# Kernel tuning notes

Measured on AMD Instinct MI355X. Metric: run time of the kernel, lower is better.

Reference implementation:

```python
import jax, jax.numpy as jnp
import numpy as np

B, H, W, C = 8, 128, 128, 384
WS, SHIFT, NH = 8, 4, 12
N = WS * WS            # tokens per window = 64
HD = C // NH           # head dim = 32
SCALE = HD ** -0.5


def _rel_pos_index():
    ch, cw = np.meshgrid(np.arange(WS), np.arange(WS), indexing='ij')
    cf = np.stack([ch.ravel(), cw.ravel()])            # (2, N)
    rel = cf[:, :, None] - cf[:, None, :]              # (2, N, N)
    rel = rel.transpose(1, 2, 0)                       # (N, N, 2)
    rel[:, :, 0] += WS - 1
    rel[:, :, 1] += WS - 1
    rel[:, :, 0] *= 2 * WS - 1
    return jnp.asarray(rel.sum(-1))                    # (N, N) int

REL_IDX = _rel_pos_index()


def _shift_mask():
    # standard Swin SW-MSA mask, built once with numpy
    img = np.zeros((1, H, W, 1), np.float32)
    cnt = 0
    for hs in (slice(0, -WS), slice(-WS, -SHIFT), slice(-SHIFT, None)):
        for ws_ in (slice(0, -WS), slice(-WS, -SHIFT), slice(-SHIFT, None)):
            img[:, hs, ws_, :] = cnt
            cnt += 1
    m = img.reshape(1, H // WS, WS, W // WS, WS, 1).transpose(0, 1, 3, 2, 4, 5)
    m = m.reshape(-1, N)                               # (nW, N)
    am = m[:, None, :] - m[:, :, None]                 # (nW, N, N)
    return np.where(am != 0, np.float32(-100.0), np.float32(0.0))


def _ln(x, g, b, eps=1e-5):
    mu = x.mean(-1, keepdims=True)
    var = ((x - mu) ** 2).mean(-1, keepdims=True)
    return (x - mu) * jax.lax.rsqrt(var + eps) * g + b


def setup_inputs() -> dict:
    key = jax.random.key(0)
    ks = jax.random.split(key, 10)
    s = 0.02
    return {
        'x': jax.random.normal(ks[0], (B, H * W, C), jnp.float32),
        'qkv_w': jax.random.normal(ks[1], (3 * C, C), jnp.float32) * s,
        'qkv_b': jnp.zeros((3 * C,), jnp.float32),
        'proj_w': jax.random.normal(ks[2], (C, C), jnp.float32) * s,
        'proj_b': jnp.zeros((C,), jnp.float32),
        'rel_bias_table': jax.random.normal(ks[3], ((2 * WS - 1) ** 2, NH), jnp.float32) * s,
        'g1': jnp.ones((C,), jnp.float32), 'b1': jnp.zeros((C,), jnp.float32),
        'g2': jnp.ones((C,), jnp.float32), 'b2': jnp.zeros((C,), jnp.float32),
        'fc1_w': jax.random.normal(ks[4], (4 * C, C), jnp.float32) * s,
        'fc1_b': jnp.zeros((4 * C,), jnp.float32),
        'fc2_w': jax.random.normal(ks[5], (C, 4 * C), jnp.float32) * s,
        'fc2_b': jnp.zeros((C,), jnp.float32),
        'attn_mask': jnp.asarray(_shift_mask()),       # (nW, N, N)
    }


def reference(x, qkv_w, qkv_b, proj_w, proj_b, rel_bias_table, g1, b1, g2, b2,
              fc1_w, fc1_b, fc2_w, fc2_b, attn_mask):
    shortcut = x
    h = _ln(x, g1, b1).reshape(B, H, W, C)
    # cyclic shift (SW-MSA)
    h = jnp.roll(h, (-SHIFT, -SHIFT), axis=(1, 2))
    # window partition -> (B*nW, N, C)
    nWh, nWw = H // WS, W // WS
    hw = h.reshape(B, nWh, WS, nWw, WS, C).transpose(0, 1, 3, 2, 4, 5)
    hw = hw.reshape(B * nWh * nWw, N, C)
    # qkv projection
    qkv = jnp.einsum('bnc,dc->bnd', hw, qkv_w) + qkv_b   # (Bw, N, 3C)
    qkv = qkv.reshape(-1, N, 3, NH, HD).transpose(2, 0, 3, 1, 4)
    q, k, v = qkv[0], qkv[1], qkv[2]                    # (Bw, NH, N, HD)
    attn = jnp.einsum('bhnd,bhmd->bhnm', q * SCALE, k)  # (Bw, NH, N, N)
    bias = rel_bias_table[REL_IDX.reshape(-1)].reshape(N, N, NH)
    attn = attn + bias.transpose(2, 0, 1)[None]
    # shift mask: attn viewed as (B, nW, NH, N, N) + mask (nW, 1, N, N)
    nW = nWh * nWw
    attn = attn.reshape(B, nW, NH, N, N) + attn_mask[None, :, None]
    attn = jax.nn.softmax(attn.reshape(-1, NH, N, N), axis=-1)
    out = jnp.einsum('bhnm,bhmd->bnhd', attn, v).reshape(-1, N, C)
    out = jnp.einsum('bnc,dc->bnd', out, proj_w) + proj_b
    # window reverse + un-shift
    out = out.reshape(B, nWh, nWw, WS, WS, C).transpose(0, 1, 3, 2, 4, 5)
    out = out.reshape(B, H, W, C)
    out = jnp.roll(out, (SHIFT, SHIFT), axis=(1, 2)).reshape(B, H * W, C)
    x = shortcut + out
    # MLP block
    h2 = _ln(x, g2, b2)
    h2 = jax.nn.gelu(jnp.einsum('blc,dc->bld', h2, fc1_w) + fc1_b, approximate=False)
    h2 = jnp.einsum('bld,cd->blc', h2, fc2_w) + fc2_b
    return x + h2
```

## Files before the change

### kernel.cpp

```cpp
#include <hip/hip_runtime.h>
#include <hip/hip_bf16.h>
#include <math.h>

typedef __attribute__((ext_vector_type(4))) float f32x4;
typedef __attribute__((ext_vector_type(8))) short bf16x8;

__device__ __forceinline__ unsigned short f2bf(float f) {
  unsigned int x = __builtin_bit_cast(unsigned int, f);
  x += 0x7fffu + ((x >> 16) & 1u);
  return (unsigned short)(x >> 16);
}

__device__ __forceinline__ void gload_lds16(const void* g, void* l) {
  __builtin_amdgcn_global_load_lds(
      (const __attribute__((address_space(1))) unsigned int*)g,
      (__attribute__((address_space(3))) unsigned int*)l, 16, 0, 0);
}

__global__ void cvt_f32_bf16(const float* __restrict__ s, unsigned short* __restrict__ d, int n) {
  int i = blockIdx.x * 256 + threadIdx.x;
  if (i < n) d[i] = f2bf(s[i]);
}

template <int REMAP>
__global__ __launch_bounds__(256)
void ln_kernel(const float* __restrict__ x, const float* __restrict__ g,
               const float* __restrict__ b, unsigned short* __restrict__ dst_o) {
  int r = blockIdx.x * 4 + (threadIdx.x >> 6);
  int lane = threadIdx.x & 63;
  size_t src;
  if (REMAP) {
    int w = r >> 6, t = r & 63;
    int bb = w >> 8, wi = (w >> 4) & 15, wj = w & 15;
    int i = t >> 3, j = t & 7;
    int p = (wi * 8 + i + 4) & 127, q = (wj * 8 + j + 4) & 127;
    src = ((size_t)bb * 16384 + p * 128 + q) * 384;
  } else {
    src = (size_t)r * 384;
  }
  float v[6];
  float s = 0.f, s2 = 0.f;
#pragma unroll
  for (int m = 0; m < 6; ++m) {
    v[m] = x[src + lane + 64 * m];
    s += v[m];
    s2 += v[m] * v[m];
  }
#pragma unroll
  for (int o2 = 1; o2 < 64; o2 <<= 1) {
    s += __shfl_xor(s, o2);
    s2 += __shfl_xor(s2, o2);
  }
  float mu = s * (1.f / 384.f);
  float var = s2 * (1.f / 384.f) - mu * mu;
  float ri = rsqrtf(var + 1e-5f);
  size_t dst = (size_t)r * 384;
#pragma unroll
  for (int m = 0; m < 6; ++m) {
    int c = lane + 64 * m;
    dst_o[dst + c] = f2bf((v[m] - mu) * ri * g[c] + b[c]);
  }
}

template <int EPI>
__global__ __launch_bounds__(256, 2)
void gemm_bt(const unsigned short* __restrict__ A, const unsigned short* __restrict__ Bw,
             const float* __restrict__ bias, int M, int N, int K,
             unsigned short* __restrict__ Obf, const float* __restrict__ resid,
             float* __restrict__ Of) {
  __shared__ unsigned short smA[128 * 64];
  __shared__ unsigned short smB[128 * 64];
  const int tid = threadIdx.x;
  const int lane = tid & 63;
  const int wid = tid >> 6;
  const int wm = wid >> 1, wn = wid & 1;
  const int li = lane & 15, lg = lane >> 4;
  const int m0 = blockIdx.y * 128;
  const int n0 = blockIdx.x * 128;

  f32x4 acc[4][4] = {};

  const int srow = wid * 32 + (lane >> 3);
  const int scol = (lane & 7) * 8;
  const unsigned short* gA = A + (size_t)(m0 + srow) * K + scol;
  const unsigned short* gB = Bw + (size_t)(n0 + srow) * K + scol;

  for (int k0 = 0; k0 < K; k0 += 64) {
#pragma unroll
    for (int c = 0; c < 4; ++c) {
      gload_lds16(gA + (size_t)(c * 8) * K + k0, &smA[(wid * 32 + c * 8) * 64]);
      gload_lds16(gB + (size_t)(c * 8) * K + k0, &smB[(wid * 32 + c * 8) * 64]);
    }
    __syncthreads();
#pragma unroll
    for (int kk = 0; kk < 2; ++kk) {
      bf16x8 a[4], bb[4];
#pragma unroll
      for (int f = 0; f < 4; ++f) {
        a[f] = *(const bf16x8*)&smA[(wm * 64 + f * 16 + li) * 64 + kk * 32 + lg * 8];
        bb[f] = *(const bf16x8*)&smB[(wn * 64 + f * 16 + li) * 64 + kk * 32 + lg * 8];
      }
#pragma unroll
      for (int mf = 0; mf < 4; ++mf)
#pragma unroll
        for (int nf = 0; nf < 4; ++nf)
          acc[mf][nf] = __builtin_amdgcn_mfma_f32_16x16x32_bf16(a[mf], bb[nf], acc[mf][nf], 0, 0, 0);
    }
    __syncthreads();
  }

#pragma unroll
  for (int mf = 0; mf < 4; ++mf) {
#pragma unroll
    for (int r = 0; r < 4; ++r) {
      int mrow = m0 + wm * 64 + mf * 16 + lg * 4 + r;
      size_t orow = (size_t)mrow;
      if (EPI == 2) {
        int w = mrow >> 6, t = mrow & 63;
        int bb2 = w >> 8, wi = (w >> 4) & 15, wj = w & 15;
        int i = t >> 3, j = t & 7;
        int p = (wi * 8 + i + 4) & 127, q = (wj * 8 + j + 4) & 127;
        orow = (size_t)bb2 * 16384 + p * 128 + q;
      }
#pragma unroll
      for (int nf = 0; nf < 4; ++nf) {
        int col = n0 + wn * 64 + nf * 16 + li;
        float v = acc[mf][nf][r] + bias[col];
        if (EPI == 0) {
          Obf[(size_t)mrow * N + col] = f2bf(v);
        } else if (EPI == 1) {
          float gl = 0.5f * v * (1.f + erff(v * 0.70710678118654752f));
          Obf[(size_t)mrow * N + col] = f2bf(gl);
        } else if (EPI == 2) {
          Of[orow * 384 + col] = v + resid[orow * 384 + col];
        } else {
          Of[(size_t)mrow * N + col] = v + resid[(size_t)mrow * N + col];
        }
      }
    }
  }
}

__global__ __launch_bounds__(256, 2)
void attn_kernel(const unsigned short* __restrict__ qkv, const float* __restrict__ btab,
                 const float* __restrict__ mask, unsigned short* __restrict__ out) {
  __shared__ unsigned short v_lds[4][64 * 40];
  __shared__ unsigned short p_lds[4][64 * 72];
  const int w = blockIdx.x;
  const int tid = threadIdx.x;
  const int wid = tid >> 6, lane = tid & 63;
  const int li = lane & 15, lg = lane >> 4;
  const float* mrow = mask + (size_t)(w & 255) * 4096;
  const size_t base = (size_t)w * 64;
  const float SC = 0.17677669529663688f;

#pragma unroll 1
  for (int hi = 0; hi < 3; ++hi) {
    int h = wid * 3 + hi;
    bf16x8 aq[4], bk[4];
#pragma unroll
    for (int f = 0; f < 4; ++f) {
      size_t off = (base + f * 16 + li) * 1152 + h * 32 + lg * 8;
      aq[f] = *(const bf16x8*)&qkv[off];
      bk[f] = *(const bf16x8*)&qkv[off + 384];
    }
    f32x4 s[4][4] = {};
#pragma unroll
    for (int mf = 0; mf < 4; ++mf)
#pragma unroll
      for (int nf = 0; nf < 4; ++nf)
        s[mf][nf] = __builtin_amdgcn_mfma_f32_16x16x32_bf16(aq[mf], bk[nf], s[mf][nf], 0, 0, 0);

    {
      const unsigned short* vp = &qkv[(base + lane) * 1152 + 768 + h * 32];
      unsigned short* dp = &v_lds[wid][lane * 40];
#pragma unroll
      for (int c = 0; c < 4; ++c) *(bf16x8*)&dp[c * 8] = *(const bf16x8*)&vp[c * 8];
    }

#pragma unroll
    for (int mf = 0; mf < 4; ++mf) {
#pragma unroll
      for (int r = 0; r < 4; ++r) {
        int m = mf * 16 + lg * 4 + r;
        float mx = -1e30f;
#pragma unroll
        for (int nf = 0; nf < 4; ++nf) {
          int n = nf * 16 + li;
          int ridx = ((m >> 3) - (n >> 3) + 7) * 15 + (m & 7) - (n & 7) + 7;
          float val = s[mf][nf][r] * SC + btab[ridx * 12 + h] + mrow[m * 64 + n];
          s[mf][nf][r] = val;
          mx = fmaxf(mx, val);
        }
#pragma unroll
        for (int o2 = 1; o2 < 16; o2 <<= 1) mx = fmaxf(mx, __shfl_xor(mx, o2));
        float sum = 0.f;
#pragma unroll
        for (int nf = 0; nf < 4; ++nf) {
          float e = __expf(s[mf][nf][r] - mx);
          s[mf][nf][r] = e;
          sum += e;
        }
#pragma unroll
        for (int o2 = 1; o2 < 16; o2 <<= 1) sum += __shfl_xor(sum, o2);
        float inv = 1.f / sum;
#pragma unroll
        for (int nf = 0; nf < 4; ++nf) s[mf][nf][r] *= inv;
      }
    }

#pragma unroll
    for (int mf = 0; mf < 4; ++mf)
#pragma unroll
      for (int nf = 0; nf < 4; ++nf)
#pragma unroll
        for (int r = 0; r < 4; ++r) {
          int m = mf * 16 + lg * 4 + r, n = nf * 16 + li;
          p_lds[wid][m * 72 + n] = f2bf(s[mf][nf][r]);
        }

    f32x4 o[4][2] = {};
#pragma unroll
    for (int kf = 0; kf < 2; ++kf) {
      bf16x8 bv[2];
#pragma unroll
      for (int df = 0; df < 2; ++df) {
        bf16x8 t;
#pragma unroll
        for (int e = 0; e < 8; ++e)
          t[e] = (short)v_lds[wid][(kf * 32 + lg * 8 + e) * 40 + df * 16 + li];
        bv[df] = t;
      }
#pragma unroll
      for (int mf = 0; mf < 4; ++mf) {
        bf16x8 pa = *(const bf16x8*)&p_lds[wid][(mf * 16 + li) * 72 + kf * 32 + lg * 8];
#pragma unroll
        for (int df = 0; df < 2; ++df)
          o[mf][df] = __builtin_amdgcn_mfma_f32_16x16x32_bf16(pa, bv[df], o[mf][df], 0, 0, 0);
      }
    }

#pragma unroll
    for (int mf = 0; mf < 4; ++mf)
#pragma unroll
      for (int df = 0; df < 2; ++df)
#pragma unroll
        for (int r = 0; r < 4; ++r) {
          size_t row = base + mf * 16 + lg * 4 + r;
          out[row * 384 + h * 32 + df * 16 + li] = f2bf(o[mf][df][r]);
        }
  }
}

extern "C" void kernel_launch(void* const* d_in, const int* in_sizes, int n_in,
                              void* d_out, int out_size, void* d_ws, size_t ws_size,
                              hipStream_t stream) {
  const float* x      = (const float*)d_in[0];
  const float* qkv_w  = (const float*)d_in[1];
  const float* qkv_b  = (const float*)d_in[2];
  const float* proj_w = (const float*)d_in[3];
  const float* proj_b = (const float*)d_in[4];
  const float* rel    = (const float*)d_in[5];
  const float* g1     = (const float*)d_in[6];
  const float* b1     = (const float*)d_in[7];
  const float* g2     = (const float*)d_in[8];
  const float* b2     = (const float*)d_in[9];
  const float* fc1_w  = (const float*)d_in[10];
  const float* fc1_b  = (const float*)d_in[11];
  const float* fc2_w  = (const float*)d_in[12];
  const float* fc2_b  = (const float*)d_in[13];
  const float* mask   = (const float*)d_in[14];
  float* out = (float*)d_out;
  char* ws = (char*)d_ws;

  const int M = 131072;
  unsigned short* hw     = (unsigned short*)ws;
  unsigned short* qkv    = (unsigned short*)(ws + 100663296);
  unsigned short* hmid   = (unsigned short*)ws;
  unsigned short* attn_o = (unsigned short*)(ws + 402653184);
  unsigned short* ln2o   = attn_o;
  float*          x1     = (float*)(ws + 503316480);
  unsigned short* wq     = (unsigned short*)(ws + 704643072);
  unsigned short* wp     = wq + 442368;
  unsigned short* w1     = wp + 147456;
  unsigned short* w2     = w1 + 589824;

  cvt_f32_bf16<<<(442368 + 255) / 256, 256, 0, stream>>>(qkv_w, wq, 442368);
  cvt_f32_bf16<<<(147456 + 255) / 256, 256, 0, stream>>>(proj_w, wp, 147456);
  cvt_f32_bf16<<<(589824 + 255) / 256, 256, 0, stream>>>(fc1_w, w1, 589824);
  cvt_f32_bf16<<<(589824 + 255) / 256, 256, 0, stream>>>(fc2_w, w2, 589824);

  ln_kernel<1><<<M / 4, 256, 0, stream>>>(x, g1, b1, hw);

  gemm_bt<0><<<dim3(9, 1024), 256, 0, stream>>>(hw, wq, qkv_b, M, 1152, 384, qkv, nullptr, nullptr);

  attn_kernel<<<2048, 256, 0, stream>>>(qkv, rel, mask, attn_o);

  gemm_bt<2><<<dim3(3, 1024), 256, 0, stream>>>(attn_o, wp, proj_b, M, 384, 384, nullptr, x, x1);

  ln_kernel<0><<<M / 4, 256, 0, stream>>>(x1, g2, b2, ln2o);

  gemm_bt<1><<<dim3(12, 1024), 256, 0, stream>>>(ln2o, w1, fc1_b, M, 1536, 384, hmid, nullptr, nullptr);

  gemm_bt<3><<<dim3(3, 1024), 256, 0, stream>>>(hmid, w2, fc2_b, M, 384, 1536, nullptr, x1, out);
}
```

Measured before the change: 1.272 ms.

## Double-buffer A tiles, read weights directly from global, remap blocks per XCD

The GEMM kernel now double-buffers only the activation tile in LDS, prefetching the next K slice while computing the current one. Weight fragments are loaded straight from global memory (through cache) instead of being staged in LDS. Launches become 1D, with the block index remapped so consecutive tiles land on the same XCD for L2 reuse. Occupancy is raised to 4 blocks/CU. There is a risk: the loop body no longer shows a __syncthreads between prefetch and compute, so buffer hazards may exist, and direct global B loads may add latency.

```diff
diff --git a/kernel.cpp b/kernel.cpp
--- a/kernel.cpp
+++ b/kernel.cpp
@@ -63,43 +63,59 @@
 }
 
 template <int EPI>
-__global__ __launch_bounds__(256, 2)
+__global__ __launch_bounds__(256, 4)
 void gemm_bt(const unsigned short* __restrict__ A, const unsigned short* __restrict__ Bw,
-             const float* __restrict__ bias, int M, int N, int K,
+             const float* __restrict__ bias, int M, int N, int K, int NT,
              unsigned short* __restrict__ Obf, const float* __restrict__ resid,
              float* __restrict__ Of) {
-  __shared__ unsigned short smA[128 * 64];
-  __shared__ unsigned short smB[128 * 64];
+  __shared__ unsigned short smA[2][128 * 64];
   const int tid = threadIdx.x;
   const int lane = tid & 63;
   const int wid = tid >> 6;
   const int wm = wid >> 1, wn = wid & 1;
   const int li = lane & 15, lg = lane >> 4;
-  const int m0 = blockIdx.y * 128;
-  const int n0 = blockIdx.x * 128;
-
-  f32x4 acc[4][4] = {};
+
+  const int nwg = gridDim.x;
+  const int orig = blockIdx.x;
+  const int q = nwg >> 3, r = nwg & 7;
+  const int xcd = orig & 7, loc = orig >> 3;
+  const int wg = (xcd < r ? xcd * (q + 1) : r * (q + 1) + (xcd - r) * q) + loc;
+  const int m0 = (wg / NT) * 128;
+  const int n0 = (wg % NT) * 128;
 
   const int srow = wid * 32 + (lane >> 3);
   const int scol = (lane & 7) * 8;
   const unsigned short* gA = A + (size_t)(m0 + srow) * K + scol;
-  const unsigned short* gB = Bw + (size_t)(n0 + srow) * K + scol;
-
-  for (int k0 = 0; k0 < K; k0 += 64) {
-#pragma unroll
-    for (int c = 0; c < 4; ++c) {
-      gload_lds16(gA + (size_t)(c * 8) * K + k0, &smA[(wid * 32 + c * 8) * 64]);
-      gload_lds16(gB + (size_t)(c * 8) * K + k0, &smB[(wid * 32 + c * 8) * 64]);
-    }
-    __syncthreads();
+  const unsigned short* gB[4];
+#pragma unroll
+  for (int nf = 0; nf < 4; ++nf)
+    gB[nf] = Bw + (size_t)(n0 + wn * 64 + nf * 16 + li) * K + lg * 8;
+
+  f32x4 acc[4][4] = {};
+  const int nk = K >> 6;
+
+#pragma unroll
+  for (int c = 0; c < 4; ++c)
+    gload_lds16(gA + (size_t)(c * 8) * K, &smA[0][(wid * 32 + c * 8) * 64]);
+  __syncthreads();
+
+  for (int k0 = 0; k0 < nk; ++k0) {
+    const int cur = k0 & 1;
+    if (k0 + 1 < nk) {
+#pragma unroll
+      for (int c = 0; c < 4; ++c)
+        gload_lds16(gA + (size_t)(c * 8) * K + (k0 + 1) * 64,
+                    &smA[cur ^ 1][(wid * 32 + c * 8) * 64]);
+    }
 #pragma unroll
     for (int kk = 0; kk < 2; ++kk) {
       bf16x8 a[4], bb[4];
 #pragma unroll
-      for (int f = 0; f < 4; ++f) {
-        a[f] = *(const bf16x8*)&smA[(wm * 64 + f * 16 + li) * 64 + kk * 32 + lg * 8];
-        bb[f] = *(const bf16x8*)&smB[(wn * 64 + f * 16 + li) * 64 + kk * 32 + lg * 8];
-      }
+      for (int f = 0; f < 4; ++f)
+        a[f] = *(const bf16x8*)&smA[cur][(wm * 64 + f * 16 + li) * 64 + kk * 32 + lg * 8];
+#pragma unroll
+      for (int f = 0; f < 4; ++f)
+        bb[f] = *(const bf16x8*)&gB[f][(size_t)(k0 * 64 + kk * 32)];
 #pragma unroll
       for (int mf = 0; mf < 4; ++mf)
 #pragma unroll
@@ -112,20 +128,20 @@
 #pragma unroll
   for (int mf = 0; mf < 4; ++mf) {
 #pragma unroll
-    for (int r = 0; r < 4; ++r) {
-      int mrow = m0 + wm * 64 + mf * 16 + lg * 4 + r;
+    for (int r2 = 0; r2 < 4; ++r2) {
+      int mrow = m0 + wm * 64 + mf * 16 + lg * 4 + r2;
       size_t orow = (size_t)mrow;
       if (EPI == 2) {
         int w = mrow >> 6, t = mrow & 63;
         int bb2 = w >> 8, wi = (w >> 4) & 15, wj = w & 15;
         int i = t >> 3, j = t & 7;
-        int p = (wi * 8 + i + 4) & 127, q = (wj * 8 + j + 4) & 127;
-        orow = (size_t)bb2 * 16384 + p * 128 + q;
+        int p = (wi * 8 + i + 4) & 127, qq = (wj * 8 + j + 4) & 127;
+        orow = (size_t)bb2 * 16384 + p * 128 + qq;
       }
 #pragma unroll
       for (int nf = 0; nf < 4; ++nf) {
         int col = n0 + wn * 64 + nf * 16 + li;
-        float v = acc[mf][nf][r] + bias[col];
+        float v = acc[mf][nf][r2] + bias[col];
         if (EPI == 0) {
           Obf[(size_t)mrow * N + col] = f2bf(v);
         } else if (EPI == 1) {
@@ -292,15 +308,15 @@
 
   ln_kernel<1><<<M / 4, 256, 0, stream>>>(x, g1, b1, hw);
 
-  gemm_bt<0><<<dim3(9, 1024), 256, 0, stream>>>(hw, wq, qkv_b, M, 1152, 384, qkv, nullptr, nullptr);
+  gemm_bt<0><<<9 * 1024, 256, 0, stream>>>(hw, wq, qkv_b, M, 1152, 384, 9, qkv, nullptr, nullptr);
 
   attn_kernel<<<2048, 256, 0, stream>>>(qkv, rel, mask, attn_o);
 
-  gemm_bt<2><<<dim3(3, 1024), 256, 0, stream>>>(attn_o, wp, proj_b, M, 384, 384, nullptr, x, x1);
+  gemm_bt<2><<<3 * 1024, 256, 0, stream>>>(attn_o, wp, proj_b, M, 384, 384, 3, nullptr, x, x1);
 
   ln_kernel<0><<<M / 4, 256, 0, stream>>>(x1, g2, b2, ln2o);
 
-  gemm_bt<1><<<dim3(12, 1024), 256, 0, stream>>>(ln2o, w1, fc1_b, M, 1536, 384, hmid, nullptr, nullptr);
-
-  gemm_bt<3><<<dim3(3, 1024), 256, 0, stream>>>(hmid, w2, fc2_b, M, 384, 1536, nullptr, x1, out);
-}
+  gemm_bt<1><<<12 * 1024, 256, 0, stream>>>(ln2o, w1, fc1_b, M, 1536, 384, 12, hmid, nullptr, nullptr);
+
+  gemm_bt<3><<<3 * 1024, 256, 0, stream>>>(hmid, w2, fc2_b, M, 384, 1536, 3, nullptr, x1, out);
+}
```

Result: slower. 1.509 ms (+18.6%).
